# Kernel optimization log

Hardware: AMD Instinct MI355X
Metric: run time of the kernel (lower is better)

The kernel has to match this reference:

```python
import jax, jax.numpy as jnp
import numpy as np

B, C_IN, C_OUT, N, T = 32, 64, 64, 1024, 16


def setup_inputs() -> dict:
    key = jax.random.key(0)
    k1, k2, k3, k4, k5 = jax.random.split(key, 5)
    x = jax.random.normal(k1, (B, C_IN, N, T), dtype=jnp.float32)
    adj = jax.random.uniform(k2, (N, N), dtype=jnp.float32)
    alpha = jax.random.normal(k3, (C_IN,), dtype=jnp.float32) * 0.1
    W_att = jax.random.normal(k4, (T, T), dtype=jnp.float32) * 0.1
    W_out = jax.random.normal(k5, (C_OUT, C_IN), dtype=jnp.float32) * 0.1
    return {"x": x, "adj": adj, "alpha": alpha, "W_att": W_att, "W_out": W_out}


def reference(x, adj, alpha, W_att, W_out):
    # x: [B, C_in, N, T]; adj: [N, N]
    # k = q = einsum('bint,i->bnt', x, alpha)
    k = jnp.einsum('bint,i->bnt', x, alpha)              # [B, N, T]
    # scores = k @ W @ q^T over timestep dim -> [B, N, N]
    scores = jnp.einsum('bnt,ts,bms->bnm', k, W_att, k)
    att = jax.nn.softmax(scores, axis=-1) * adj          # [B, N, N]
    # out = (att @ x.permute(3,0,2,1)) @ W_out.T, then permute back
    agg = jnp.einsum('bnm,bcmt->bcnt', att, x)           # [B, C_in, N, T]
    out = jnp.einsum('bcnt,oc->bont', agg, W_out)        # [B, C_out, N, T]
    return out
```

## Files before the change

### kernel.cpp

```cpp
#include <hip/hip_runtime.h>
#include <hip/hip_bf16.h>


typedef float  f32x4 __attribute__((ext_vector_type(4)));
typedef short  s16x8 __attribute__((ext_vector_type(8)));
typedef unsigned short u16x8 __attribute__((ext_vector_type(8)));

#define GLOAD_LDS16(g, l) __builtin_amdgcn_global_load_lds(                    \
    (const __attribute__((address_space(1))) void*)(g),                        \
    (__attribute__((address_space(3))) void*)(l), 16, 0, 0)

static __device__ __forceinline__ unsigned short f2bf(float f) {
    __hip_bfloat16 h = __float2bfloat16(f);
    return *reinterpret_cast<unsigned short*>(&h);
}

__global__ __launch_bounds__(256, 3) void kCM(const float* __restrict__ x,
                                              const float* __restrict__ Wout,
                                              const float* __restrict__ alpha,
                                              const float* __restrict__ Watt,
                                              unsigned short* __restrict__ Yt,
                                              float* __restrict__ kk_,
                                              float* __restrict__ kq_) {
    extern __shared__ char sm[];
    unsigned short* xtb = (unsigned short*)sm;
    unsigned short* Ys  = (unsigned short*)sm;
    unsigned short* Wb  = (unsigned short*)(sm + 36864);
    float* al   = (float*)(sm + 46080);
    float* wl   = (float*)(sm + 46336);
    float* kl   = (float*)(sm + 47424);
    float* kred = (float*)(sm + 48448);
    int tid = threadIdx.x;
    int b  = blockIdx.x >> 6;
    int mc = blockIdx.x & 63;
    int j0 = mc << 8;
    int m0 = mc << 4;
    int g = tid >> 6, lane = tid & 63;
    if (tid < 64) al[tid] = alpha[tid];
    wl[(tid >> 4) * 17 + (tid & 15)] = Watt[tid];
    #pragma unroll
    for (int it = 0; it < 16; ++it) {
        int idx = it * 256 + tid;
        Wb[(idx >> 6) * 72 + (idx & 63)] = f2bf(Wout[idx]);
    }
    __syncthreads();
    const float* xb = x + (size_t)b * (64 * 16384) + j0;
    float kp[4] = {0.f, 0.f, 0.f, 0.f};
    #pragma unroll
    for (int it = 0; it < 16; ++it) {
        int c = it * 4 + g;
        float4 v = *(const float4*)(xb + (size_t)c * 16384 + lane * 4);
        float a = al[c];
        kp[0] = fmaf(a, v.x, kp[0]);
        kp[1] = fmaf(a, v.y, kp[1]);
        kp[2] = fmaf(a, v.z, kp[2]);
        kp[3] = fmaf(a, v.w, kp[3]);
        ushort4 pk = make_ushort4(f2bf(v.x), f2bf(v.y), f2bf(v.z), f2bf(v.w));
        *(ushort4*)&xtb[c * 264 + lane * 4] = pk;
    }
    *(float4*)&kred[g * 256 + lane * 4] = make_float4(kp[0], kp[1], kp[2], kp[3]);
    __syncthreads();
    int l15 = lane & 15, lhi = lane >> 4;
    int jw = g << 6;
    s16x8 af[4][2], bfv[4][2];
    #pragma unroll
    for (int fro = 0; fro < 4; ++fro)
        #pragma unroll
        for (int ks = 0; ks < 2; ++ks)
            af[fro][ks] = *(const s16x8*)&Wb[(fro * 16 + l15) * 72 + ks * 32 + lhi * 8];
    #pragma unroll
    for (int fc = 0; fc < 4; ++fc)
        #pragma unroll
        for (int ks = 0; ks < 2; ++ks) {
            int jcol = jw + fc * 16 + l15;
            int cb = ks * 32 + lhi * 8;
            s16x8 t;
            #pragma unroll
            for (int e = 0; e < 8; ++e)
                t[e] = (short)xtb[(cb + e) * 264 + jcol];
            bfv[fc][ks] = t;
        }
    float kv = kred[tid] + kred[256 + tid] + kred[512 + tid] + kred[768 + tid];
    kl[tid] = kv;
    kk_[(size_t)b * 16384 + j0 + tid] = kv;
    __syncthreads();
    f32x4 acc[4][4] = {};
    #pragma unroll
    for (int ks = 0; ks < 2; ++ks)
        #pragma unroll
        for (int fc = 0; fc < 4; ++fc)
            #pragma unroll
            for (int fro = 0; fro < 4; ++fro)
                acc[fro][fc] = __builtin_amdgcn_mfma_f32_16x16x32_bf16(
                    af[fro][ks], bfv[fc][ks], acc[fro][fc], 0, 0, 0);
    {
        int ml = tid >> 4, tq = tid & 15;
        float q = 0.f;
        #pragma unroll
        for (int s = 0; s < 16; ++s) q = fmaf(kl[ml * 16 + s], wl[s * 17 + tq], q);
        kq_[(size_t)b * 16384 + j0 + tid] = q;
    }
    #pragma unroll
    for (int fro = 0; fro < 4; ++fro)
        #pragma unroll
        for (int fc = 0; fc < 4; ++fc) {
            int jl = jw + fc * 16 + l15;
            int o0 = fro * 16 + lhi * 4;
            ushort4 pk = make_ushort4(f2bf(acc[fro][fc][0]), f2bf(acc[fro][fc][1]),
                                      f2bf(acc[fro][fc][2]), f2bf(acc[fro][fc][3]));
            *(ushort4*)&Ys[jl * 72 + o0] = pk;
        }
    __syncthreads();
    #pragma unroll
    for (int it = 0; it < 4; ++it) {
        int r = it * 256 + tid;
        int o = r >> 4, t = r & 15;
        u16x8 v0, v1;
        #pragma unroll
        for (int q = 0; q < 8; ++q) {
            v0[q] = Ys[(q * 16 + t) * 72 + o];
            v1[q] = Ys[((q + 8) * 16 + t) * 72 + o];
        }
        unsigned short* dst = Yt + (((size_t)b << 10) + r) * 1024 + m0;
        *(u16x8*)dst = v0;
        *(u16x8*)(dst + 8) = v1;
    }
}

__global__ __launch_bounds__(256) void kBP(const float* __restrict__ kk_,
                                           const float* __restrict__ kq_,
                                           const float* __restrict__ adj,
                                           unsigned short* __restrict__ Pbf) {
    int tid = threadIdx.x;
    int b  = blockIdx.x >> 8;
    int n0 = (blockIdx.x & 255) * 4;
    __shared__ float kql[4][16];
    __shared__ float redm[4][4], reds[4][4];
    if (tid < 64)
        kql[tid >> 4][tid & 15] =
            kq_[((size_t)b * 1024 + n0 + (tid >> 4)) * 16 + (tid & 15)];
    __syncthreads();
    const float* kb = kk_ + (size_t)b * 16384;
    float kf[4][16];
    #pragma unroll
    for (int u = 0; u < 4; ++u) {
        const float* p = &kb[(size_t)(u * 256 + tid) * 16];
        #pragma unroll
        for (int s = 0; s < 16; ++s) kf[u][s] = p[s];
    }
    float sc[4][4];
    #pragma unroll
    for (int r = 0; r < 4; ++r)
        #pragma unroll
        for (int u = 0; u < 4; ++u) {
            float a = 0.f;
            #pragma unroll
            for (int s = 0; s < 16; ++s) a = fmaf(kql[r][s], kf[u][s], a);
            sc[r][u] = a;
        }
    float mx[4];
    #pragma unroll
    for (int r = 0; r < 4; ++r)
        mx[r] = fmaxf(fmaxf(sc[r][0], sc[r][1]), fmaxf(sc[r][2], sc[r][3]));
    #pragma unroll
    for (int off = 32; off; off >>= 1)
        #pragma unroll
        for (int r = 0; r < 4; ++r) mx[r] = fmaxf(mx[r], __shfl_xor(mx[r], off));
    int w = tid >> 6;
    if ((tid & 63) == 0)
        #pragma unroll
        for (int r = 0; r < 4; ++r) redm[w][r] = mx[r];
    __syncthreads();
    #pragma unroll
    for (int r = 0; r < 4; ++r)
        mx[r] = fmaxf(fmaxf(redm[0][r], redm[1][r]), fmaxf(redm[2][r], redm[3][r]));
    float e[4][4], se[4];
    #pragma unroll
    for (int r = 0; r < 4; ++r) {
        float s = 0.f;
        #pragma unroll
        for (int u = 0; u < 4; ++u) { e[r][u] = __expf(sc[r][u] - mx[r]); s += e[r][u]; }
        se[r] = s;
    }
    #pragma unroll
    for (int off = 32; off; off >>= 1)
        #pragma unroll
        for (int r = 0; r < 4; ++r) se[r] += __shfl_xor(se[r], off);
    if ((tid & 63) == 0)
        #pragma unroll
        for (int r = 0; r < 4; ++r) reds[w][r] = se[r];
    __syncthreads();
    float rrs[4];
    #pragma unroll
    for (int r = 0; r < 4; ++r)
        rrs[r] = 1.f / (reds[0][r] + reds[1][r] + reds[2][r] + reds[3][r]);
    #pragma unroll
    for (int r = 0; r < 4; ++r)
        #pragma unroll
        for (int u = 0; u < 4; ++u) {
            size_t m = (size_t)u * 256 + tid;
            float av = adj[(size_t)(n0 + r) * 1024 + m];
            Pbf[((size_t)b * 1024 + n0 + r) * 1024 + m] = f2bf(e[r][u] * rrs[r] * av);
        }
}

static __device__ __forceinline__ void stage_tile(const unsigned short* Pb,
                                                  const unsigned short* Yb,
                                                  unsigned short* lds, int buf,
                                                  int kt, int ww, int l) {
    int r8  = (l >> 3) & 7;
    int glc = ((l & 7) ^ r8) << 3;
    int k0  = kt << 6;
    unsigned short* base = lds + buf * 32768;
    #pragma unroll
    for (int s = 0; s < 4; ++s) {
        int row  = s * 64 + ww * 8;
        size_t g = ((size_t)(row + r8) << 10) + k0 + glc;
        GLOAD_LDS16(Pb + g, base + row * 64);
        GLOAD_LDS16(Yb + g, base + 16384 + row * 64);
    }
}

static __device__ __forceinline__ s16x8 frag_ld(const unsigned short* base,
                                                int R, int kc, int l7) {
    return *(const s16x8*)(base + R * 64 + ((kc ^ l7) << 3));
}

__global__ __launch_bounds__(512, 2) void kD(const unsigned short* __restrict__ P,
                                             const unsigned short* __restrict__ Yt,
                                             float* __restrict__ out) {
    extern __shared__ unsigned short lds[];
    int bid = blockIdx.x;
    int wg  = (bid & 7) * 64 + (bid >> 3);
    int b   = wg >> 4;
    int rem = wg & 15;
    int n0  = (rem & 3) << 8;
    int j0  = (rem >> 2) << 8;
    int tid = threadIdx.x;
    int l = tid & 63, ww = tid >> 6;
    int wr = ww >> 2, wc = ww & 3;
    int l15 = l & 15, lhi = l >> 4, l7 = l & 7;
    const unsigned short* Pb = P  + ((size_t)b << 20) + ((size_t)n0 << 10);
    const unsigned short* Yb = Yt + ((size_t)b << 20) + ((size_t)j0 << 10);

    f32x4 acc[8][4] = {};
    stage_tile(Pb, Yb, lds, 0, 0, ww, l);
    __syncthreads();

    for (int kt = 0; kt < 16; ++kt) {
        int cur = kt & 1;
        const unsigned short* Ab = lds + cur * 32768;
        const unsigned short* Bb = Ab + 16384;
        s16x8 bf[4][2];
        #pragma unroll
        for (int q = 0; q < 4; ++q) {
            if (q == 0) {
                int ktn = kt < 15 ? kt + 1 : 15;
                stage_tile(Pb, Yb, lds, cur ^ 1, ktn, ww, l);
                #pragma unroll
                for (int nj = 0; nj < 4; ++nj)
                    #pragma unroll
                    for (int ks = 0; ks < 2; ++ks)
                        bf[nj][ks] = frag_ld(Bb, wc * 64 + nj * 16 + l15,
                                             ks * 4 + lhi, l7);
            }
            s16x8 af[2][2];
            #pragma unroll
            for (int mi = 0; mi < 2; ++mi)
                #pragma unroll
                for (int ks = 0; ks < 2; ++ks)
                    af[mi][ks] = frag_ld(Ab, wr * 128 + (q * 2 + mi) * 16 + l15,
                                         ks * 4 + lhi, l7);
            __builtin_amdgcn_s_barrier();
            asm volatile("s_waitcnt lgkmcnt(0)" ::: "memory");
            __builtin_amdgcn_sched_barrier(0);
            __builtin_amdgcn_s_setprio(1);
            #pragma unroll
            for (int mi = 0; mi < 2; ++mi)
                #pragma unroll
                for (int nj = 0; nj < 4; ++nj)
                    #pragma unroll
                    for (int ks = 0; ks < 2; ++ks)
                        acc[q * 2 + mi][nj] = __builtin_amdgcn_mfma_f32_16x16x32_bf16(
                            af[mi][ks], bf[nj][ks], acc[q * 2 + mi][nj], 0, 0, 0);
            __builtin_amdgcn_s_setprio(0);
            if (q < 3) __builtin_amdgcn_s_barrier();
        }
        __syncthreads();
    }

    #pragma unroll
    for (int mi = 0; mi < 8; ++mi)
        #pragma unroll
        for (int nj = 0; nj < 4; ++nj) {
            int o  = (j0 >> 4) + wc * 4 + nj;
            int nb = n0 + wr * 128 + mi * 16 + lhi * 4;
            float* op = out + ((size_t)(b * 64 + o) << 14) + (size_t)nb * 16 + l15;
            #pragma unroll
            for (int q = 0; q < 4; ++q) op[q * 16] = acc[mi][nj][q];
        }
}

extern "C" void kernel_launch(void* const* d_in, const int* in_sizes, int n_in,
                              void* d_out, int out_size, void* d_ws, size_t ws_size,
                              hipStream_t stream) {
    const float* x     = (const float*)d_in[0];
    const float* adj   = (const float*)d_in[1];
    const float* alpha = (const float*)d_in[2];
    const float* Watt  = (const float*)d_in[3];
    const float* Wout  = (const float*)d_in[4];
    float* out = (float*)d_out;

    char* ws = (char*)d_ws;
    float* k  = (float*)ws;
    float* kq = (float*)(ws + 2097152);
    unsigned short* Pbf = (unsigned short*)(ws + 4194304);
    unsigned short* Yt  = (unsigned short*)(ws + 4194304 + 67108864);

    kCM<<<2048, 256, 52544, stream>>>(x, Wout, alpha, Watt, Yt, k, kq);
    kBP<<<8192, 256, 0, stream>>>(k, kq, adj, Pbf);
    kD <<<512, 512, 131072, stream>>>(Pbf, Yt, out);
}
```

Baseline: 193.8 us.

## Halve kCM tile with transposed LDS staging and restructure kD prefetch wait

kCM now processes 128 columns per block instead of 256. Each thread gathers 8 channels and writes them transposed into LDS, so MFMA B-fragments load as contiguous 16-byte vectors instead of strided scalar reads. The smaller LDS footprint allows a higher occupancy hint and twice as many blocks. In kD, the next tile's global-to-LDS prefetch is issued at the top of each iteration with a partial vmcnt wait and plain barriers instead of __syncthreads, which aims to overlap loads with compute but depends on the exact outstanding-load count being correct.

```diff
diff --git a/kernel.cpp b/kernel.cpp
--- a/kernel.cpp
+++ b/kernel.cpp
@@ -15,7 +15,7 @@
     return *reinterpret_cast<unsigned short*>(&h);
 }
 
-__global__ __launch_bounds__(256, 3) void kCM(const float* __restrict__ x,
+__global__ __launch_bounds__(256, 4) void kCM(const float* __restrict__ x,
                                               const float* __restrict__ Wout,
                                               const float* __restrict__ alpha,
                                               const float* __restrict__ Watt,
@@ -23,19 +23,18 @@
                                               float* __restrict__ kk_,
                                               float* __restrict__ kq_) {
     extern __shared__ char sm[];
-    unsigned short* xtb = (unsigned short*)sm;
-    unsigned short* Ys  = (unsigned short*)sm;
-    unsigned short* Wb  = (unsigned short*)(sm + 36864);
-    float* al   = (float*)(sm + 46080);
-    float* wl   = (float*)(sm + 46336);
-    float* kl   = (float*)(sm + 47424);
-    float* kred = (float*)(sm + 48448);
+    unsigned short* xtbT = (unsigned short*)sm;
+    unsigned short* Ys   = (unsigned short*)sm;
+    unsigned short* Wb   = (unsigned short*)(sm + 18432);
+    float* al   = (float*)(sm + 27648);
+    float* wl   = (float*)(sm + 27904);
+    float* kl   = (float*)(sm + 28992);
+    float* kred = (float*)(sm + 29504);
     int tid = threadIdx.x;
-    int b  = blockIdx.x >> 6;
-    int mc = blockIdx.x & 63;
-    int j0 = mc << 8;
-    int m0 = mc << 4;
-    int g = tid >> 6, lane = tid & 63;
+    int b  = blockIdx.x >> 7;
+    int mc = blockIdx.x & 127;
+    int j0 = mc << 7;
+    int m0 = mc << 3;
     if (tid < 64) al[tid] = alpha[tid];
     wl[(tid >> 4) * 17 + (tid & 15)] = Watt[tid];
     #pragma unroll
@@ -44,56 +43,64 @@
         Wb[(idx >> 6) * 72 + (idx & 63)] = f2bf(Wout[idx]);
     }
     __syncthreads();
-    const float* xb = x + (size_t)b * (64 * 16384) + j0;
-    float kp[4] = {0.f, 0.f, 0.f, 0.f};
-    #pragma unroll
-    for (int it = 0; it < 16; ++it) {
-        int c = it * 4 + g;
-        float4 v = *(const float4*)(xb + (size_t)c * 16384 + lane * 4);
+    int jq = tid & 31, cg = tid >> 5;
+    const float* xb = x + (size_t)b * (64 * 16384) + j0 + jq * 4;
+    float kp0 = 0.f, kp1 = 0.f, kp2 = 0.f, kp3 = 0.f;
+    unsigned short sh[8][4];
+    #pragma unroll
+    for (int cc = 0; cc < 8; ++cc) {
+        int c = cg * 8 + cc;
+        float4 v = *(const float4*)(xb + (size_t)c * 16384);
         float a = al[c];
-        kp[0] = fmaf(a, v.x, kp[0]);
-        kp[1] = fmaf(a, v.y, kp[1]);
-        kp[2] = fmaf(a, v.z, kp[2]);
-        kp[3] = fmaf(a, v.w, kp[3]);
-        ushort4 pk = make_ushort4(f2bf(v.x), f2bf(v.y), f2bf(v.z), f2bf(v.w));
-        *(ushort4*)&xtb[c * 264 + lane * 4] = pk;
-    }
-    *(float4*)&kred[g * 256 + lane * 4] = make_float4(kp[0], kp[1], kp[2], kp[3]);
-    __syncthreads();
-    int l15 = lane & 15, lhi = lane >> 4;
-    int jw = g << 6;
-    s16x8 af[4][2], bfv[4][2];
+        kp0 = fmaf(a, v.x, kp0); kp1 = fmaf(a, v.y, kp1);
+        kp2 = fmaf(a, v.z, kp2); kp3 = fmaf(a, v.w, kp3);
+        sh[cc][0] = f2bf(v.x); sh[cc][1] = f2bf(v.y);
+        sh[cc][2] = f2bf(v.z); sh[cc][3] = f2bf(v.w);
+    }
+    #pragma unroll
+    for (int jj = 0; jj < 4; ++jj) {
+        int j = jq * 4 + jj;
+        #pragma unroll
+        for (int h = 0; h < 2; ++h) {
+            ushort4 pk = make_ushort4(sh[h * 4 + 0][jj], sh[h * 4 + 1][jj],
+                                      sh[h * 4 + 2][jj], sh[h * 4 + 3][jj]);
+            *(ushort4*)&xtbT[j * 72 + cg * 8 + h * 4] = pk;
+        }
+    }
+    *(float4*)&kred[cg * 128 + jq * 4] = make_float4(kp0, kp1, kp2, kp3);
+    __syncthreads();
+    int w = tid >> 6, l = tid & 63;
+    int l15 = l & 15, lhi = l >> 4;
+    int jw = w << 5;
+    s16x8 af[4][2], bfv[2][2];
     #pragma unroll
     for (int fro = 0; fro < 4; ++fro)
         #pragma unroll
         for (int ks = 0; ks < 2; ++ks)
             af[fro][ks] = *(const s16x8*)&Wb[(fro * 16 + l15) * 72 + ks * 32 + lhi * 8];
     #pragma unroll
-    for (int fc = 0; fc < 4; ++fc)
-        #pragma unroll
-        for (int ks = 0; ks < 2; ++ks) {
-            int jcol = jw + fc * 16 + l15;
-            int cb = ks * 32 + lhi * 8;
-            s16x8 t;
-            #pragma unroll
-            for (int e = 0; e < 8; ++e)
-                t[e] = (short)xtb[(cb + e) * 264 + jcol];
-            bfv[fc][ks] = t;
-        }
-    float kv = kred[tid] + kred[256 + tid] + kred[512 + tid] + kred[768 + tid];
-    kl[tid] = kv;
-    kk_[(size_t)b * 16384 + j0 + tid] = kv;
-    __syncthreads();
-    f32x4 acc[4][4] = {};
+    for (int fc = 0; fc < 2; ++fc)
+        #pragma unroll
+        for (int ks = 0; ks < 2; ++ks)
+            bfv[fc][ks] = *(const s16x8*)&xtbT[(jw + fc * 16 + l15) * 72 + ks * 32 + lhi * 8];
+    if (tid < 128) {
+        float kv = 0.f;
+        #pragma unroll
+        for (int g = 0; g < 8; ++g) kv += kred[g * 128 + tid];
+        kl[tid] = kv;
+        kk_[(size_t)b * 16384 + j0 + tid] = kv;
+    }
+    __syncthreads();
+    f32x4 acc[4][2] = {};
     #pragma unroll
     for (int ks = 0; ks < 2; ++ks)
         #pragma unroll
-        for (int fc = 0; fc < 4; ++fc)
+        for (int fc = 0; fc < 2; ++fc)
             #pragma unroll
             for (int fro = 0; fro < 4; ++fro)
                 acc[fro][fc] = __builtin_amdgcn_mfma_f32_16x16x32_bf16(
                     af[fro][ks], bfv[fc][ks], acc[fro][fc], 0, 0, 0);
-    {
+    if (tid < 128) {
         int ml = tid >> 4, tq = tid & 15;
         float q = 0.f;
         #pragma unroll
@@ -103,7 +110,7 @@
     #pragma unroll
     for (int fro = 0; fro < 4; ++fro)
         #pragma unroll
-        for (int fc = 0; fc < 4; ++fc) {
+        for (int fc = 0; fc < 2; ++fc) {
             int jl = jw + fc * 16 + l15;
             int o0 = fro * 16 + lhi * 4;
             ushort4 pk = make_ushort4(f2bf(acc[fro][fc][0]), f2bf(acc[fro][fc][1]),
@@ -115,15 +122,11 @@
     for (int it = 0; it < 4; ++it) {
         int r = it * 256 + tid;
         int o = r >> 4, t = r & 15;
-        u16x8 v0, v1;
-        #pragma unroll
-        for (int q = 0; q < 8; ++q) {
-            v0[q] = Ys[(q * 16 + t) * 72 + o];
-            v1[q] = Ys[((q + 8) * 16 + t) * 72 + o];
-        }
+        u16x8 v0;
+        #pragma unroll
+        for (int q = 0; q < 8; ++q) v0[q] = Ys[(q * 16 + t) * 72 + o];
         unsigned short* dst = Yt + (((size_t)b << 10) + r) * 1024 + m0;
         *(u16x8*)dst = v0;
-        *(u16x8*)(dst + 8) = v1;
     }
 }
 
@@ -245,18 +248,22 @@
 
     f32x4 acc[8][4] = {};
     stage_tile(Pb, Yb, lds, 0, 0, ww, l);
-    __syncthreads();
 
     for (int kt = 0; kt < 16; ++kt) {
         int cur = kt & 1;
         const unsigned short* Ab = lds + cur * 32768;
         const unsigned short* Bb = Ab + 16384;
+        if (kt < 15) {
+            stage_tile(Pb, Yb, lds, cur ^ 1, kt + 1, ww, l);
+            asm volatile("s_waitcnt vmcnt(8)" ::: "memory");
+        } else {
+            asm volatile("s_waitcnt vmcnt(0)" ::: "memory");
+        }
+        __builtin_amdgcn_s_barrier();
         s16x8 bf[4][2];
         #pragma unroll
         for (int q = 0; q < 4; ++q) {
             if (q == 0) {
-                int ktn = kt < 15 ? kt + 1 : 15;
-                stage_tile(Pb, Yb, lds, cur ^ 1, ktn, ww, l);
                 #pragma unroll
                 for (int nj = 0; nj < 4; ++nj)
                     #pragma unroll
@@ -286,16 +293,17 @@
             __builtin_amdgcn_s_setprio(0);
             if (q < 3) __builtin_amdgcn_s_barrier();
         }
-        __syncthreads();
-    }
-
+        __builtin_amdgcn_s_barrier();
+    }
+
+    int t = l15;
     #pragma unroll
     for (int mi = 0; mi < 8; ++mi)
         #pragma unroll
         for (int nj = 0; nj < 4; ++nj) {
             int o  = (j0 >> 4) + wc * 4 + nj;
             int nb = n0 + wr * 128 + mi * 16 + lhi * 4;
-            float* op = out + ((size_t)(b * 64 + o) << 14) + (size_t)nb * 16 + l15;
+            float* op = out + ((size_t)(b * 64 + o) << 14) + (size_t)nb * 16 + t;
             #pragma unroll
             for (int q = 0; q < 4; ++q) op[q * 16] = acc[mi][nj][q];
         }
@@ -317,7 +325,7 @@
     unsigned short* Pbf = (unsigned short*)(ws + 4194304);
     unsigned short* Yt  = (unsigned short*)(ws + 4194304 + 67108864);
 
-    kCM<<<2048, 256, 52544, stream>>>(x, Wout, alpha, Watt, Yt, k, kq);
+    kCM<<<4096, 256, 33600, stream>>>(x, Wout, alpha, Watt, Yt, k, kq);
     kBP<<<8192, 256, 0, stream>>>(k, kq, adj, Pbf);
     kD <<<512, 512, 131072, stream>>>(Pbf, Yt, out);
 }
```

Result: slower. 215.4 us (+11.1%).
